# Performance work log

Hardware: AMD Instinct MI355X
Metric: run time of the kernel (lower is better)

Reference implementation:

```python
import jax, jax.numpy as jnp
import numpy as np

N = 100000   # nodes
E = 1600000  # edges
R = 500      # relation types
D = 128      # in_ent_feats == out_ent_feats
H = 8        # heads
Dh = 16      # head dim
DFF = 4 * D  # feed-forward hidden
HOPS = 5
ALPHA = 0.15
SLOPE = 0.2
EPS = 1e-5


def setup_inputs() -> dict:
    key = jax.random.key(0)
    ks = jax.random.split(key, 12)
    s = 0.05  # small-init scale
    return {
        "ent_feat": jax.random.normal(ks[0], (N, D), jnp.float32),
        "rel_feat": jax.random.normal(ks[1], (R, D), jnp.float32),
        "src": jax.random.randint(ks[2], (E,), 0, N),
        "dst": jax.random.randint(ks[3], (E,), 0, N),
        "e_type": jax.random.randint(ks[4], (E,), 0, R),
        "ln1_g": jnp.ones((D,), jnp.float32),
        "ln1_b": jnp.zeros((D,), jnp.float32),
        "W_ent": jax.random.normal(ks[5], (D, H * Dh), jnp.float32) * s,
        "W_rel": jax.random.normal(ks[6], (D, H * Dh), jnp.float32) * s,
        "attn_h": jax.random.normal(ks[7], (1, H, Dh), jnp.float32) * s,
        "attn_t": jax.random.normal(ks[8], (1, H, Dh), jnp.float32) * s,
        "attn_r": jax.random.normal(ks[9], (1, H, Dh), jnp.float32) * s,
        "ln2_g": jnp.ones((H * Dh,), jnp.float32),
        "ln2_b": jnp.zeros((H * Dh,), jnp.float32),
        "W1": jax.random.normal(ks[10], (H * Dh, DFF), jnp.float32) * s,
        "b1": jnp.zeros((DFF,), jnp.float32),
        "W2": jax.random.normal(ks[11], (DFF, H * Dh), jnp.float32) * s,
        "b2": jnp.zeros((H * Dh,), jnp.float32),
    }


def _ln(x, g, b):
    mu = x.mean(-1, keepdims=True)
    var = x.var(-1, keepdims=True)
    return (x - mu) * jax.lax.rsqrt(var + EPS) * g + b


def reference(ent_feat, rel_feat, src, dst, e_type,
              ln1_g, ln1_b, W_ent, W_rel, attn_h, attn_t, attn_r,
              ln2_g, ln2_b, W1, b1, W2, b2):
    # graph layer norm (dropout is identity at eval)
    h = _ln(ent_feat, ln1_g, ln1_b)                       # [N, D]
    feat = (h @ W_ent).reshape(N, H, Dh)                  # [N, H, Dh]
    frel = (rel_feat @ W_rel).reshape(R, H, Dh)           # [R, H, Dh]
    eh = (feat * attn_h).sum(-1)                          # [N, H]
    et = (feat * attn_t).sum(-1)                          # [N, H]
    er = (frel * attn_r).sum(-1)[e_type]                  # [E, H]
    # edge scores: u_add_v + relation term, leaky relu
    e = eh[src] + et[dst] + er                            # [E, H]
    e = jnp.where(e > 0, e, SLOPE * e)
    # edge softmax over incoming edges of each dst node
    m = jax.ops.segment_max(e, dst, num_segments=N)       # [N, H]
    ex = jnp.exp(e - m[dst])
    ssum = jax.ops.segment_sum(ex, dst, num_segments=N)
    a = ex / ssum[dst]                                    # [E, H]
    # PPR diffusion
    feat0 = feat
    f = feat0
    for _ in range(HOPS):
        msg = f[src] * a[:, :, None]                      # [E, H, Dh]
        agg = jax.ops.segment_sum(msg, dst, num_segments=N)
        f = (1.0 - ALPHA) * agg + ALPHA * feat0
    # residual (Identity since in == out)
    rst = f + h.reshape(N, H, Dh)
    rst = rst.reshape(N, H * Dh)
    # feed-forward sublayer with residual
    y = _ln(rst, ln2_g, ln2_b)
    ff = jax.nn.relu(y @ W1 + b1) @ W2 + b2
    return ff + rst
```

## Files before the change

kernel.cpp:

```cpp
#include <hip/hip_runtime.h>
#include <hip/hip_bf16.h>
#include <math.h>

#define N_NODES 100000
#define N_EDGES 1600000
#define N_REL   500
#define DIM     128
#define NHEAD   8
#define DFF     512
#define ALPHA   0.15f
#define SLOPE   0.2f
#define LN_EPS  1e-5f

#define SCHUNK   1024
#define NSCANBLK ((N_NODES + SCHUNK - 1) / SCHUNK)

#define NWIN    8
#define WNODES  12500
#define NECHUNK 256
#define ECHUNK  (N_EDGES / NECHUNK)

typedef unsigned short u16;
typedef unsigned int   u32;

typedef __attribute__((ext_vector_type(8))) short  bf16x8;
typedef __attribute__((ext_vector_type(4))) float  f32x4;

__device__ __forceinline__ float bf2f(u16 u) {
    return __uint_as_float(((u32)u) << 16);
}
__device__ __forceinline__ u16 f2bf(float f) {
    __hip_bfloat16 b = __float2bfloat16(f);
    return *reinterpret_cast<u16*>(&b);
}

__global__ void zero_k(int* __restrict__ p, int n) {
    int i = blockIdx.x * blockDim.x + threadIdx.x;
    if (i < n) p[i] = 0;
}

__global__ void swz1_k(const float* __restrict__ W1, u16* __restrict__ W1s) {
    const int i = blockIdx.x * 256 + threadIdx.x;
    const int k = i >> 9, n = i & 511;
    W1s[n * DIM + k] = f2bf(W1[i]);
}
__global__ void swz2_k(const float* __restrict__ W2, u16* __restrict__ W2s) {
    const int i = blockIdx.x * 256 + threadIdx.x;
    const int k = i >> 7, n = i & 127;
    W2s[n * DFF + k] = f2bf(W2[i]);
}
__global__ void swze_k(const float* __restrict__ W, u16* __restrict__ Ws) {
    const int i = blockIdx.x * 256 + threadIdx.x;
    const int k = i >> 7, n = i & 127;
    Ws[n * DIM + k] = f2bf(W[i]);
}

__global__ __launch_bounds__(128) void ln1_k(const float* __restrict__ x,
        const float* __restrict__ g, const float* __restrict__ b,
        float* __restrict__ h) {
    const int n = blockIdx.x, t = threadIdx.x;
    const float v = x[n * DIM + t];
    float s = v, q = v * v;
#pragma unroll
    for (int off = 32; off > 0; off >>= 1) {
        s += __shfl_xor(s, off, 64);
        q += __shfl_xor(q, off, 64);
    }
    __shared__ float ss[2], qq[2];
    if ((t & 63) == 0) { ss[t >> 6] = s; qq[t >> 6] = q; }
    __syncthreads();
    s = ss[0] + ss[1]; q = qq[0] + qq[1];
    const float mu  = s * (1.0f / 128.0f);
    const float var = q * (1.0f / 128.0f) - mu * mu;
    const float rs  = rsqrtf(fmaxf(var, 0.f) + LN_EPS);
    h[n * DIM + t] = (v - mu) * rs * g[t] + b[t];
}

#define HP 136
__global__ __launch_bounds__(256) void proj_k(const float* __restrict__ h,
        const u16* __restrict__ Wes,
        u16* __restrict__ feat0) {
    __shared__ u16 hsb[32 * HP];
    const int t   = threadIdx.x;
    const int n0b = blockIdx.x * 32;

    {
        const int sr = t >> 3;
        const int sc = (t & 7) * 16;
        const float* hrow = &h[(size_t)(n0b + sr) * DIM + sc];
        u16* drow = &hsb[sr * HP + sc];
#pragma unroll
        for (int i = 0; i < 4; ++i) {
            const float4 hv = ((const float4*)hrow)[i];
            ushort4 o;
            o.x = f2bf(hv.x); o.y = f2bf(hv.y); o.z = f2bf(hv.z); o.w = f2bf(hv.w);
            ((ushort4*)drow)[i] = o;
        }
    }
    __syncthreads();

    const int wv   = t >> 6;
    const int lane = t & 63;
    const int lm   = lane & 15;
    const int q4   = lane >> 4;
    const int mrow = (wv & 1) * 16;
    const int chalf = (wv >> 1) * 64;

    bf16x8 afr[4];
#pragma unroll
    for (int kt = 0; kt < 4; ++kt)
        afr[kt] = *(const bf16x8*)&hsb[(mrow + lm) * HP + kt * 32 + q4 * 8];

#pragma unroll
    for (int nt = 0; nt < 4; ++nt) {
        const int c0 = chalf + nt * 16;
        f32x4 acc = {0.f, 0.f, 0.f, 0.f};
#pragma unroll
        for (int kt = 0; kt < 4; ++kt) {
            const bf16x8 bfr = *(const bf16x8*)&Wes[(c0 + lm) * DIM + kt * 32 + q4 * 8];
            acc = __builtin_amdgcn_mfma_f32_16x16x32_bf16(afr[kt], bfr, acc, 0, 0, 0);
        }
#pragma unroll
        for (int r = 0; r < 4; ++r)
            feat0[(size_t)(n0b + mrow + q4 * 4 + r) * DIM + c0 + lm] = f2bf(acc[r]);
    }
}

__global__ __launch_bounds__(256) void eh_k(const u16* __restrict__ feat0,
        const float* __restrict__ attn_h, const float* __restrict__ attn_t,
        float* __restrict__ eh, float* __restrict__ et) {
    __shared__ float ahs[DIM], ats[DIM];
    const int t = threadIdx.x;
    if (t < DIM) { ahs[t] = attn_h[t]; ats[t] = attn_t[t]; }
    __syncthreads();
    const int idx  = blockIdx.x * 256 + t;
    const int n    = idx >> 3;
    const int head = idx & 7;
    const u16* fp = &feat0[(size_t)n * DIM + head * 16];
    float sh = 0.f, st = 0.f;
#pragma unroll
    for (int i = 0; i < 4; ++i) {
        const ushort4 f4 = ((const ushort4*)fp)[i];
        const int c = head * 16 + i * 4;
        sh += bf2f(f4.x) * ahs[c+0] + bf2f(f4.y) * ahs[c+1]
            + bf2f(f4.z) * ahs[c+2] + bf2f(f4.w) * ahs[c+3];
        st += bf2f(f4.x) * ats[c+0] + bf2f(f4.y) * ats[c+1]
            + bf2f(f4.z) * ats[c+2] + bf2f(f4.w) * ats[c+3];
    }
    eh[idx] = sh;
    et[idx] = st;
}

__global__ __launch_bounds__(128) void rel_k(const float* __restrict__ rel_feat,
        const float* __restrict__ W,
        const float* __restrict__ attn_r, float* __restrict__ er) {
    __shared__ float rf[DIM];
    __shared__ float pr[DIM];
    const int r = blockIdx.x, t = threadIdx.x;
    rf[t] = rel_feat[r * DIM + t];
    __syncthreads();
    float acc = 0.f;
    for (int d = 0; d < DIM; ++d) acc += rf[d] * W[d * DIM + t];
    pr[t] = acc * attn_r[t];
    __syncthreads();
    if (t < NHEAD) {
        float s = 0.f;
        for (int i = 0; i < 16; ++i) s += pr[t * 16 + i];
        er[r * NHEAD + t] = s;
    }
}

__global__ void count_k(const int* __restrict__ dst, int* __restrict__ counts) {
    int e = blockIdx.x * blockDim.x + threadIdx.x;
    if (e < N_EDGES) atomicAdd(&counts[dst[e]], 1);
}

__global__ __launch_bounds__(256) void scan1_k(const int* __restrict__ counts,
        int* __restrict__ offsets, int* __restrict__ blk_sums, int n) {
    __shared__ int wsum[4];
    const int t = threadIdx.x, lane = t & 63, wid = t >> 6;
    const int base = blockIdx.x * SCHUNK + t * 4;
    int v0 = 0, v1 = 0, v2 = 0, v3 = 0;
    if (base + 3 < n) {
        const int4 c4 = *(const int4*)&counts[base];
        v0 = c4.x; v1 = c4.y; v2 = c4.z; v3 = c4.w;
    } else {
        if (base + 0 < n) v0 = counts[base + 0];
        if (base + 1 < n) v1 = counts[base + 1];
        if (base + 2 < n) v2 = counts[base + 2];
        if (base + 3 < n) v3 = counts[base + 3];
    }
    const int s4 = v0 + v1 + v2 + v3;
    int incl = s4;
#pragma unroll
    for (int off = 1; off < 64; off <<= 1) {
        const int tt = __shfl_up(incl, off, 64);
        if (lane >= off) incl += tt;
    }
    if (lane == 63) wsum[wid] = incl;
    __syncthreads();
    int wbase = 0;
#pragma unroll
    for (int w = 0; w < 4; ++w) if (w < wid) wbase += wsum[w];
    const int excl = wbase + incl - s4;
    if (base + 0 < n) offsets[base + 0] = excl;
    if (base + 1 < n) offsets[base + 1] = excl + v0;
    if (base + 2 < n) offsets[base + 2] = excl + v0 + v1;
    if (base + 3 < n) offsets[base + 3] = excl + v0 + v1 + v2;
    if (t == 255) blk_sums[blockIdx.x] = wbase + incl;
}

__global__ __launch_bounds__(128) void scan2_k(const int* __restrict__ blk_sums,
        int* __restrict__ blk_off, int* __restrict__ offsets, int nblk, int n) {
    const int t = threadIdx.x;
    const int v = (t < nblk) ? blk_sums[t] : 0;
    int incl = v;
#pragma unroll
    for (int off = 1; off < 64; off <<= 1) {
        const int tt = __shfl_up(incl, off, 64);
        if ((t & 63) >= off) incl += tt;
    }
    __shared__ int w0sum;
    if (t == 63) w0sum = incl;
    __syncthreads();
    int x = incl - v;
    if (t >= 64) x += w0sum;
    if (t < nblk) blk_off[t] = x;
    if (t == nblk - 1) offsets[n] = x + v;
}

__global__ __launch_bounds__(256) void scan3_k(int* __restrict__ offsets,
        int* __restrict__ cursor, const int* __restrict__ blk_off, int n) {
    const int add  = blk_off[blockIdx.x];
    const int base = blockIdx.x * SCHUNK + threadIdx.x * 4;
#pragma unroll
    for (int j = 0; j < 4; ++j) {
        const int i = base + j;
        if (i < n) {
            const int o = offsets[i] + add;
            offsets[i] = o;
            cursor[i]  = o;
        }
    }
}

__global__ __launch_bounds__(256) void scatter_k(const int* __restrict__ src,
        const int* __restrict__ dst, const int* __restrict__ etype,
        int* __restrict__ cursor, u32* __restrict__ csr_se) {
    const int b  = blockIdx.x;
    const int w  = b & (NWIN - 1);
    const int r  = b >> 3;
    const int lo = w * WNODES, hi = lo + WNODES;
    const int base = r * ECHUNK;
    for (int i = threadIdx.x; i < ECHUNK; i += 256) {
        const int e = base + i;
        const int d = dst[e];
        if (d >= lo && d < hi) {
            const int s   = src[e];
            const int rel = etype[e];
            const int pos = atomicAdd(&cursor[d], 1);
            if (pos >= 0 && pos < N_EDGES)
                csr_se[pos] = (u32)s | ((u32)rel << 17);
        }
    }
}

__global__ __launch_bounds__(256) void softmax_k(const int* __restrict__ offsets,
        const u32* __restrict__ csr_se,
        const float* __restrict__ eh, const float* __restrict__ et,
        const float* __restrict__ er,
        u16* __restrict__ csr_ab, float* __restrict__ inv_buf) {
    const int n = blockIdx.x * 4 + (threadIdx.x >> 6);
    const int beg = offsets[n], end = offsets[n + 1];
    const int lane = threadIdx.x & 63;
    const int k  = lane & 7;
    const int eo = lane >> 3;
    const float etk = et[n * NHEAD + k];
    float m = -1e30f;
    for (int e = beg + eo; e < end; e += 8) {
        const u32 se = csr_se[e];
        const int s = se & 0x1FFFF;
        const int r = se >> 17;
        float sc = eh[s * NHEAD + k] + etk + er[r * NHEAD + k];
        sc = sc > 0.f ? sc : SLOPE * sc;
        m = fmaxf(m, sc);
    }
    m = fmaxf(m, __shfl_xor(m, 8, 64));
    m = fmaxf(m, __shfl_xor(m, 16, 64));
    m = fmaxf(m, __shfl_xor(m, 32, 64));
    float ssum = 0.f;
    for (int e = beg + eo; e < end; e += 8) {
        const u32 se = csr_se[e];
        const int s = se & 0x1FFFF;
        const int r = se >> 17;
        float sc = eh[s * NHEAD + k] + etk + er[r * NHEAD + k];
        sc = sc > 0.f ? sc : SLOPE * sc;
        const float ex = expf(sc - m);
        csr_ab[(size_t)e * NHEAD + k] = f2bf(ex);
        ssum += ex;
    }
    ssum += __shfl_xor(ssum, 8, 64);
    ssum += __shfl_xor(ssum, 16, 64);
    ssum += __shfl_xor(ssum, 32, 64);
    const float inv = 1.f / fmaxf(ssum, 1e-20f);
    if (lane < 8) inv_buf[n * NHEAD + lane] = inv;
}

__global__ __launch_bounds__(256) void hop_k(const u16* __restrict__ f_in,
        u16* __restrict__ f_out, const u16* __restrict__ feat0,
        const int* __restrict__ offsets, const u32* __restrict__ csr_se,
        const u16* __restrict__ csr_ab, const float* __restrict__ inv_buf) {
    const int n    = blockIdx.x * 4 + (threadIdx.x >> 6);
    const int lane = threadIdx.x & 63;
    const int li   = lane & 15;
    const int grp  = lane >> 4;
    const int hsel = li >> 1;
    const int beg = offsets[n], end = offsets[n + 1];

    float acc[8];
#pragma unroll
    for (int j = 0; j < 8; ++j) acc[j] = 0.f;

    int e0 = beg;
    for (; e0 + 32 <= end; e0 += 32) {
        const u32 seA = csr_se[e0 + li];
        const u32 seB = csr_se[e0 + 16 + li];
        bf16x8 row[8];
        float  a[8];
#pragma unroll
        for (int u = 0; u < 4; ++u) {
            const int s = (int)(__shfl(seA, u * 4 + grp, 16) & 0x1FFFF);
            row[u] = *(const bf16x8*)&f_in[(size_t)s * DIM + li * 8];
            a[u]   = bf2f(csr_ab[(size_t)(e0 + u * 4 + grp) * NHEAD + hsel]);
        }
#pragma unroll
        for (int u = 0; u < 4; ++u) {
            const int s = (int)(__shfl(seB, u * 4 + grp, 16) & 0x1FFFF);
            row[4 + u] = *(const bf16x8*)&f_in[(size_t)s * DIM + li * 8];
            a[4 + u]   = bf2f(csr_ab[(size_t)(e0 + 16 + u * 4 + grp) * NHEAD + hsel]);
        }
#pragma unroll
        for (int u = 0; u < 8; ++u)
#pragma unroll
            for (int j = 0; j < 8; ++j)
                acc[j] += a[u] * bf2f((u16)row[u][j]);
    }
    for (; e0 + 16 <= end; e0 += 16) {
        const u32 se16 = csr_se[e0 + li];
#pragma unroll
        for (int u = 0; u < 4; ++u) {
            const int eu = e0 + u * 4 + grp;
            const int s  = (int)(__shfl(se16, u * 4 + grp, 16) & 0x1FFFF);
            const float av = bf2f(csr_ab[(size_t)eu * NHEAD + hsel]);
            const bf16x8 rw = *(const bf16x8*)&f_in[(size_t)s * DIM + li * 8];
#pragma unroll
            for (int j = 0; j < 8; ++j)
                acc[j] += av * bf2f((u16)rw[j]);
        }
    }
    for (int e = e0 + grp; e < end; e += 4) {
        const u32 se = csr_se[e];
        const int s  = (int)(se & 0x1FFFF);
        const float av = bf2f(csr_ab[(size_t)e * NHEAD + hsel]);
        const bf16x8 rw = *(const bf16x8*)&f_in[(size_t)s * DIM + li * 8];
#pragma unroll
        for (int j = 0; j < 8; ++j)
            acc[j] += av * bf2f((u16)rw[j]);
    }
#pragma unroll
    for (int j = 0; j < 8; ++j) {
        acc[j] += __shfl_xor(acc[j], 16, 64);
        acc[j] += __shfl_xor(acc[j], 32, 64);
    }
    if (lane < 16) {
        const float iv = inv_buf[n * NHEAD + hsel];
        const bf16x8 p = *(const bf16x8*)&feat0[(size_t)n * DIM + li * 8];
        bf16x8 o;
#pragma unroll
        for (int j = 0; j < 8; ++j)
            o[j] = (short)f2bf((1.f - ALPHA) * acc[j] * iv + ALPHA * bf2f((u16)p[j]));
        *(bf16x8*)&f_out[(size_t)n * DIM + li * 8] = o;
    }
}

#define YP 136
#define ZP 520
__global__ __launch_bounds__(256) void ffn_k(const u16* __restrict__ f,
        const float* __restrict__ h,
        const float* __restrict__ g2, const float* __restrict__ b2ln,
        const u16* __restrict__ W1s,
        const float* __restrict__ b1,
        const u16* __restrict__ W2s,
        const float* __restrict__ b2,
        float* __restrict__ out) {
    __shared__ u16 ysb[32 * YP];
    __shared__ u16 zsb[32 * ZP];
    __shared__ float red[32][8];
    __shared__ float red2[32][8];
    __shared__ float mu_s[32], rs_s[32];

    const int t   = threadIdx.x;
    const int n0b = blockIdx.x * 32;

    const int an = t >> 3;
    const int ap = t & 7;
    float rv[16];
    {
        const int gbase = (n0b + an) * DIM + ap * 16;
#pragma unroll
        for (int i = 0; i < 4; ++i) {
            const ushort4 fu = *(const ushort4*)&f[gbase + i * 4];
            const float4  hv = *(const float4*)&h[gbase + i * 4];
            rv[i * 4 + 0] = bf2f(fu.x) + hv.x;
            rv[i * 4 + 1] = bf2f(fu.y) + hv.y;
            rv[i * 4 + 2] = bf2f(fu.z) + hv.z;
            rv[i * 4 + 3] = bf2f(fu.w) + hv.w;
        }
        float s = 0.f, q = 0.f;
#pragma unroll
        for (int i = 0; i < 16; ++i) { s += rv[i]; q += rv[i] * rv[i]; }
        red[an][ap] = s; red2[an][ap] = q;
    }
    __syncthreads();
    if (t < 32) {
        float s = 0.f, q = 0.f;
#pragma unroll
        for (int i = 0; i < 8; ++i) { s += red[t][i]; q += red2[t][i]; }
        const float mu  = s * (1.0f / 128.0f);
        const float var = q * (1.0f / 128.0f) - mu * mu;
        mu_s[t] = mu;
        rs_s[t] = rsqrtf(fmaxf(var, 0.f) + LN_EPS);
    }
    __syncthreads();
    {
        const float mu = mu_s[an], rs = rs_s[an];
#pragma unroll
        for (int i = 0; i < 4; ++i) {
            ushort4 yo;
            const int c = ap * 16 + i * 4;
            yo.x = f2bf((rv[i*4+0] - mu) * rs * g2[c+0] + b2ln[c+0]);
            yo.y = f2bf((rv[i*4+1] - mu) * rs * g2[c+1] + b2ln[c+1]);
            yo.z = f2bf((rv[i*4+2] - mu) * rs * g2[c+2] + b2ln[c+2]);
            yo.w = f2bf((rv[i*4+3] - mu) * rs * g2[c+3] + b2ln[c+3]);
            *(ushort4*)&ysb[an * YP + c] = yo;
        }
    }
    __syncthreads();

    const int wv   = t >> 6;
    const int lane = t & 63;
    const int lm   = lane & 15;
    const int q4   = lane >> 4;

    bf16x8 afr[2][4];
#pragma unroll
    for (int mt = 0; mt < 2; ++mt)
#pragma unroll
        for (int kt = 0; kt < 4; ++kt)
            afr[mt][kt] = *(const bf16x8*)&ysb[(mt * 16 + lm) * YP + kt * 32 + q4 * 8];

    for (int nt = 0; nt < 8; ++nt) {
        const int n0 = wv * 128 + nt * 16;
        f32x4 acc0 = {0.f, 0.f, 0.f, 0.f};
        f32x4 acc1 = {0.f, 0.f, 0.f, 0.f};
#pragma unroll
        for (int kt = 0; kt < 4; ++kt) {
            const bf16x8 bfr = *(const bf16x8*)&W1s[(n0 + lm) * DIM + kt * 32 + q4 * 8];
            acc0 = __builtin_amdgcn_mfma_f32_16x16x32_bf16(afr[0][kt], bfr, acc0, 0, 0, 0);
            acc1 = __builtin_amdgcn_mfma_f32_16x16x32_bf16(afr[1][kt], bfr, acc1, 0, 0, 0);
        }
        const float bias = b1[n0 + lm];
#pragma unroll
        for (int r = 0; r < 4; ++r) {
            zsb[(q4 * 4 + r) * ZP + n0 + lm]        = f2bf(fmaxf(acc0[r] + bias, 0.f));
            zsb[(16 + q4 * 4 + r) * ZP + n0 + lm]   = f2bf(fmaxf(acc1[r] + bias, 0.f));
        }
    }
    __syncthreads();

    f32x4 acc[2][2];
#pragma unroll
    for (int i = 0; i < 2; ++i)
#pragma unroll
        for (int j = 0; j < 2; ++j)
            acc[i][j] = (f32x4){0.f, 0.f, 0.f, 0.f};
    const int c0 = wv * 32;
    for (int kt = 0; kt < 16; ++kt) {
        const bf16x8 a0 = *(const bf16x8*)&zsb[(lm) * ZP + kt * 32 + q4 * 8];
        const bf16x8 a1 = *(const bf16x8*)&zsb[(16 + lm) * ZP + kt * 32 + q4 * 8];
        const bf16x8 b0 = *(const bf16x8*)&W2s[(c0 + lm) * DFF + kt * 32 + q4 * 8];
        const bf16x8 b1f = *(const bf16x8*)&W2s[(c0 + 16 + lm) * DFF + kt * 32 + q4 * 8];
        acc[0][0] = __builtin_amdgcn_mfma_f32_16x16x32_bf16(a0, b0, acc[0][0], 0, 0, 0);
        acc[0][1] = __builtin_amdgcn_mfma_f32_16x16x32_bf16(a0, b1f, acc[0][1], 0, 0, 0);
        acc[1][0] = __builtin_amdgcn_mfma_f32_16x16x32_bf16(a1, b0, acc[1][0], 0, 0, 0);
        acc[1][1] = __builtin_amdgcn_mfma_f32_16x16x32_bf16(a1, b1f, acc[1][1], 0, 0, 0);
    }

#pragma unroll
    for (int ntile = 0; ntile < 2; ++ntile) {
        const int col = c0 + ntile * 16 + lm;
        const float bias = b2[col];
#pragma unroll
        for (int mt = 0; mt < 2; ++mt) {
#pragma unroll
            for (int r = 0; r < 4; ++r) {
                const int row  = mt * 16 + q4 * 4 + r;
                const int gidx = (n0b + row) * DIM + col;
                out[gidx] = acc[mt][ntile][r] + bias + bf2f(f[gidx]) + h[gidx];
            }
        }
    }
}

extern "C" void kernel_launch(void* const* d_in, const int* in_sizes, int n_in,
                              void* d_out, int out_size, void* d_ws, size_t ws_size,
                              hipStream_t stream) {
    const float* ent_feat = (const float*)d_in[0];
    const float* rel_feat = (const float*)d_in[1];
    const int*   src      = (const int*)d_in[2];
    const int*   dst      = (const int*)d_in[3];
    const int*   e_type   = (const int*)d_in[4];
    const float* ln1_g    = (const float*)d_in[5];
    const float* ln1_b    = (const float*)d_in[6];
    const float* W_ent    = (const float*)d_in[7];
    const float* W_rel    = (const float*)d_in[8];
    const float* attn_h   = (const float*)d_in[9];
    const float* attn_t   = (const float*)d_in[10];
    const float* attn_r   = (const float*)d_in[11];
    const float* ln2_g    = (const float*)d_in[12];
    const float* ln2_b    = (const float*)d_in[13];
    const float* W1       = (const float*)d_in[14];
    const float* b1       = (const float*)d_in[15];
    const float* W2       = (const float*)d_in[16];
    const float* b2       = (const float*)d_in[17];
    float* out = (float*)d_out;

    char* ws = (char*)d_ws;
    size_t used = 0;
    auto alloc = [&](size_t bytes) -> char* {
        char* p = ws + used;
        used += (bytes + 255) & ~(size_t)255;
        return p;
    };
    float* h       = (float*)alloc((size_t)N_NODES * DIM * 4);
    u16*   feat0   = (u16*)  alloc((size_t)N_NODES * DIM * 2);
    u16*   fA      = (u16*)  alloc((size_t)N_NODES * DIM * 2);
    u16*   fB      = (u16*)  alloc((size_t)N_NODES * DIM * 2);
    u16*   csr_ab  = (u16*)  alloc((size_t)N_EDGES * NHEAD * 2);
    float* eh      = (float*)alloc((size_t)N_NODES * NHEAD * 4);
    float* et      = (float*)alloc((size_t)N_NODES * NHEAD * 4);
    float* inv_buf = (float*)alloc((size_t)N_NODES * NHEAD * 4);
    u32*   csr_se  = (u32*)  alloc((size_t)N_EDGES * 4);
    int*   counts  = (int*)  alloc((size_t)N_NODES * 4);
    int*   offsets = (int*)  alloc((size_t)(N_NODES + 1) * 4);
    int*   cursor  = (int*)  alloc((size_t)N_NODES * 4);
    float* er      = (float*)alloc((size_t)N_REL * NHEAD * 4);
    u16*   W1s     = (u16*)  alloc((size_t)DIM * DFF * 2);
    u16*   W2s     = (u16*)  alloc((size_t)DFF * DIM * 2);
    u16*   Wes     = (u16*)  alloc((size_t)DIM * DIM * 2);
    int*   blk_sums= (int*)  alloc((size_t)NSCANBLK * 4);
    int*   blk_off = (int*)  alloc((size_t)NSCANBLK * 4);

    if (used > ws_size) return;

    swz1_k<<<DIM * DFF / 256, 256, 0, stream>>>(W1, W1s);
    swz2_k<<<DFF * DIM / 256, 256, 0, stream>>>(W2, W2s);
    swze_k<<<DIM * DIM / 256, 256, 0, stream>>>(W_ent, Wes);

    ln1_k<<<N_NODES, 128, 0, stream>>>(ent_feat, ln1_g, ln1_b, h);
    proj_k<<<N_NODES / 32, 256, 0, stream>>>(h, Wes, feat0);
    eh_k<<<N_NODES * NHEAD / 256, 256, 0, stream>>>(feat0, attn_h, attn_t, eh, et);
    rel_k<<<N_REL, 128, 0, stream>>>(rel_feat, W_rel, attn_r, er);

    zero_k<<<(N_NODES + 255) / 256, 256, 0, stream>>>(counts, N_NODES);
    count_k<<<(N_EDGES + 255) / 256, 256, 0, stream>>>(dst, counts);
    scan1_k<<<NSCANBLK, 256, 0, stream>>>(counts, offsets, blk_sums, N_NODES);
    scan2_k<<<1, 128, 0, stream>>>(blk_sums, blk_off, offsets, NSCANBLK, N_NODES);
    scan3_k<<<NSCANBLK, 256, 0, stream>>>(offsets, cursor, blk_off, N_NODES);
    scatter_k<<<NECHUNK * NWIN, 256, 0, stream>>>(src, dst, e_type,
                                                  cursor, csr_se);
    softmax_k<<<N_NODES / 4, 256, 0, stream>>>(offsets, csr_se, eh, et, er,
                                               csr_ab, inv_buf);

    hop_k<<<N_NODES / 4, 256, 0, stream>>>(feat0, fA, feat0, offsets, csr_se, csr_ab, inv_buf);
    hop_k<<<N_NODES / 4, 256, 0, stream>>>(fA, fB, feat0, offsets, csr_se, csr_ab, inv_buf);
    hop_k<<<N_NODES / 4, 256, 0, stream>>>(fB, fA, feat0, offsets, csr_se, csr_ab, inv_buf);
    hop_k<<<N_NODES / 4, 256, 0, stream>>>(fA, fB, feat0, offsets, csr_se, csr_ab, inv_buf);
    hop_k<<<N_NODES / 4, 256, 0, stream>>>(fB, fA, feat0, offsets, csr_se, csr_ab, inv_buf);

    ffn_k<<<N_NODES / 32, 256, 0, stream>>>(fA, h, ln2_g, ln2_b, W1s, b1, W2s, b2,
                                            out);
}
```

Before: 936.1 us.

## Cache softmax scores, simplify hop gather loop, prefetch FFN weights, shuffle-reduce LN

Softmax now keeps the first four per-lane edge scores in registers, so the common low-degree case skips reloading and recomputing them in the exp pass. The hop kernel replaces its 32/16/tail loops with a single 16-edge loop that predicates the ragged tail. It also sets launch_bounds to 8 blocks for more occupancy and unpacks bf16 pairs directly with bit ops. The FFN kernel replaces the shared-memory LayerNorm reduction and two barriers with wave shuffles, and double-buffers W1/W2 fragment loads ahead of the MFMAs. The risks are register pressure from the occupancy hint and prefetch buffers, and less memory-level parallelism per wave in the hop gather.

```diff
diff --git a/kernel.cpp b/kernel.cpp
--- a/kernel.cpp
+++ b/kernel.cpp
@@ -32,6 +32,15 @@
 __device__ __forceinline__ u16 f2bf(float f) {
     __hip_bfloat16 b = __float2bfloat16(f);
     return *reinterpret_cast<u16*>(&b);
+}
+
+__device__ __forceinline__ void fma_row(float* acc, float a, const bf16x8& r) {
+    const u32* w = (const u32*)&r;
+#pragma unroll
+    for (int jj = 0; jj < 4; ++jj) {
+        acc[2 * jj]     += a * __uint_as_float(w[jj] << 16);
+        acc[2 * jj + 1] += a * __uint_as_float(w[jj] & 0xffff0000u);
+    }
 }
 
 __global__ void zero_k(int* __restrict__ p, int n) {
@@ -276,26 +285,38 @@
     const int k  = lane & 7;
     const int eo = lane >> 3;
     const float etk = et[n * NHEAD + k];
-    float m = -1e30f;
-    for (int e = beg + eo; e < end; e += 8) {
+
+    auto score = [&](int e) -> float {
         const u32 se = csr_se[e];
         const int s = se & 0x1FFFF;
         const int r = se >> 17;
         float sc = eh[s * NHEAD + k] + etk + er[r * NHEAD + k];
-        sc = sc > 0.f ? sc : SLOPE * sc;
-        m = fmaxf(m, sc);
-    }
+        return sc > 0.f ? sc : SLOPE * sc;
+    };
+
+    const int e0 = beg + eo;
+    float c0 = 0.f, c1 = 0.f, c2 = 0.f, c3 = 0.f;
+    float m = -1e30f;
+    if (e0 < end)      { c0 = score(e0);      m = fmaxf(m, c0); }
+    if (e0 + 8 < end)  { c1 = score(e0 + 8);  m = fmaxf(m, c1); }
+    if (e0 + 16 < end) { c2 = score(e0 + 16); m = fmaxf(m, c2); }
+    if (e0 + 24 < end) { c3 = score(e0 + 24); m = fmaxf(m, c3); }
+    for (int e = e0 + 32; e < end; e += 8) m = fmaxf(m, score(e));
     m = fmaxf(m, __shfl_xor(m, 8, 64));
     m = fmaxf(m, __shfl_xor(m, 16, 64));
     m = fmaxf(m, __shfl_xor(m, 32, 64));
+
     float ssum = 0.f;
-    for (int e = beg + eo; e < end; e += 8) {
-        const u32 se = csr_se[e];
-        const int s = se & 0x1FFFF;
-        const int r = se >> 17;
-        float sc = eh[s * NHEAD + k] + etk + er[r * NHEAD + k];
-        sc = sc > 0.f ? sc : SLOPE * sc;
-        const float ex = expf(sc - m);
+    if (e0 < end)      { const float ex = expf(c0 - m);
+                         csr_ab[(size_t)e0 * NHEAD + k] = f2bf(ex); ssum += ex; }
+    if (e0 + 8 < end)  { const float ex = expf(c1 - m);
+                         csr_ab[(size_t)(e0 + 8) * NHEAD + k] = f2bf(ex); ssum += ex; }
+    if (e0 + 16 < end) { const float ex = expf(c2 - m);
+                         csr_ab[(size_t)(e0 + 16) * NHEAD + k] = f2bf(ex); ssum += ex; }
+    if (e0 + 24 < end) { const float ex = expf(c3 - m);
+                         csr_ab[(size_t)(e0 + 24) * NHEAD + k] = f2bf(ex); ssum += ex; }
+    for (int e = e0 + 32; e < end; e += 8) {
+        const float ex = expf(score(e) - m);
         csr_ab[(size_t)e * NHEAD + k] = f2bf(ex);
         ssum += ex;
     }
@@ -306,7 +327,7 @@
     if (lane < 8) inv_buf[n * NHEAD + lane] = inv;
 }
 
-__global__ __launch_bounds__(256) void hop_k(const u16* __restrict__ f_in,
+__global__ __launch_bounds__(256, 8) void hop_k(const u16* __restrict__ f_in,
         u16* __restrict__ f_out, const u16* __restrict__ feat0,
         const int* __restrict__ offsets, const u32* __restrict__ csr_se,
         const u16* __restrict__ csr_ab, const float* __restrict__ inv_buf) {
@@ -321,51 +342,42 @@
 #pragma unroll
     for (int j = 0; j < 8; ++j) acc[j] = 0.f;
 
-    int e0 = beg;
-    for (; e0 + 32 <= end; e0 += 32) {
-        const u32 seA = csr_se[e0 + li];
-        const u32 seB = csr_se[e0 + 16 + li];
-        bf16x8 row[8];
-        float  a[8];
-#pragma unroll
-        for (int u = 0; u < 4; ++u) {
-            const int s = (int)(__shfl(seA, u * 4 + grp, 16) & 0x1FFFF);
-            row[u] = *(const bf16x8*)&f_in[(size_t)s * DIM + li * 8];
-            a[u]   = bf2f(csr_ab[(size_t)(e0 + u * 4 + grp) * NHEAD + hsel]);
-        }
-#pragma unroll
-        for (int u = 0; u < 4; ++u) {
-            const int s = (int)(__shfl(seB, u * 4 + grp, 16) & 0x1FFFF);
-            row[4 + u] = *(const bf16x8*)&f_in[(size_t)s * DIM + li * 8];
-            a[4 + u]   = bf2f(csr_ab[(size_t)(e0 + 16 + u * 4 + grp) * NHEAD + hsel]);
-        }
-#pragma unroll
-        for (int u = 0; u < 8; ++u)
-#pragma unroll
-            for (int j = 0; j < 8; ++j)
-                acc[j] += a[u] * bf2f((u16)row[u][j]);
-    }
-    for (; e0 + 16 <= end; e0 += 16) {
-        const u32 se16 = csr_se[e0 + li];
-#pragma unroll
-        for (int u = 0; u < 4; ++u) {
-            const int eu = e0 + u * 4 + grp;
-            const int s  = (int)(__shfl(se16, u * 4 + grp, 16) & 0x1FFFF);
-            const float av = bf2f(csr_ab[(size_t)eu * NHEAD + hsel]);
-            const bf16x8 rw = *(const bf16x8*)&f_in[(size_t)s * DIM + li * 8];
-#pragma unroll
-            for (int j = 0; j < 8; ++j)
-                acc[j] += av * bf2f((u16)rw[j]);
-        }
-    }
-    for (int e = e0 + grp; e < end; e += 4) {
-        const u32 se = csr_se[e];
-        const int s  = (int)(se & 0x1FFFF);
-        const float av = bf2f(csr_ab[(size_t)e * NHEAD + hsel]);
-        const bf16x8 rw = *(const bf16x8*)&f_in[(size_t)s * DIM + li * 8];
-#pragma unroll
-        for (int j = 0; j < 8; ++j)
-            acc[j] += av * bf2f((u16)rw[j]);
+    for (int e0 = beg; e0 < end; e0 += 16) {
+        const u32 se16 = csr_se[min(e0 + li, end - 1)];
+        const int s0 = (int)(__shfl(se16, grp,      16) & 0x1FFFF);
+        const int s1 = (int)(__shfl(se16, 4 + grp,  16) & 0x1FFFF);
+        const int s2 = (int)(__shfl(se16, 8 + grp,  16) & 0x1FFFF);
+        const int s3 = (int)(__shfl(se16, 12 + grp, 16) & 0x1FFFF);
+        if (e0 + 16 <= end) {
+            const bf16x8 r0 = *(const bf16x8*)&f_in[(size_t)s0 * DIM + li * 8];
+            const bf16x8 r1 = *(const bf16x8*)&f_in[(size_t)s1 * DIM + li * 8];
+            const bf16x8 r2 = *(const bf16x8*)&f_in[(size_t)s2 * DIM + li * 8];
+            const bf16x8 r3 = *(const bf16x8*)&f_in[(size_t)s3 * DIM + li * 8];
+            const float a0 = bf2f(csr_ab[(size_t)(e0 + grp)      * NHEAD + hsel]);
+            const float a1 = bf2f(csr_ab[(size_t)(e0 + 4 + grp)  * NHEAD + hsel]);
+            const float a2 = bf2f(csr_ab[(size_t)(e0 + 8 + grp)  * NHEAD + hsel]);
+            const float a3 = bf2f(csr_ab[(size_t)(e0 + 12 + grp) * NHEAD + hsel]);
+            fma_row(acc, a0, r0);
+            fma_row(acc, a1, r1);
+            fma_row(acc, a2, r2);
+            fma_row(acc, a3, r3);
+        } else {
+            const int rem = end - e0;
+            bf16x8 r0 = {}, r1 = {}, r2 = {}, r3 = {};
+            float a0 = 0.f, a1 = 0.f, a2 = 0.f, a3 = 0.f;
+            if (grp < rem)      { r0 = *(const bf16x8*)&f_in[(size_t)s0 * DIM + li * 8];
+                                  a0 = bf2f(csr_ab[(size_t)(e0 + grp)      * NHEAD + hsel]); }
+            if (grp + 4 < rem)  { r1 = *(const bf16x8*)&f_in[(size_t)s1 * DIM + li * 8];
+                                  a1 = bf2f(csr_ab[(size_t)(e0 + 4 + grp)  * NHEAD + hsel]); }
+            if (grp + 8 < rem)  { r2 = *(const bf16x8*)&f_in[(size_t)s2 * DIM + li * 8];
+                                  a2 = bf2f(csr_ab[(size_t)(e0 + 8 + grp)  * NHEAD + hsel]); }
+            if (grp + 12 < rem) { r3 = *(const bf16x8*)&f_in[(size_t)s3 * DIM + li * 8];
+                                  a3 = bf2f(csr_ab[(size_t)(e0 + 12 + grp) * NHEAD + hsel]); }
+            fma_row(acc, a0, r0);
+            fma_row(acc, a1, r1);
+            fma_row(acc, a2, r2);
+            fma_row(acc, a3, r3);
+        }
     }
 #pragma unroll
     for (int j = 0; j < 8; ++j) {
@@ -395,18 +407,18 @@
         float* __restrict__ out) {
     __shared__ u16 ysb[32 * YP];
     __shared__ u16 zsb[32 * ZP];
-    __shared__ float red[32][8];
-    __shared__ float red2[32][8];
-    __shared__ float mu_s[32], rs_s[32];
-
-    const int t   = threadIdx.x;
-    const int n0b = blockIdx.x * 32;
-
-    const int an = t >> 3;
-    const int ap = t & 7;
-    float rv[16];
+
+    const int t    = threadIdx.x;
+    const int n0b  = blockIdx.x * 32;
+    const int wv   = t >> 6;
+    const int lane = t & 63;
+
     {
-        const int gbase = (n0b + an) * DIM + ap * 16;
+        const int nl   = lane >> 3;
+        const int node = wv * 8 + nl;
+        const int cp   = (lane & 7) * 16;
+        const int gbase = (n0b + node) * DIM + cp;
+        float rv[16];
 #pragma unroll
         for (int i = 0; i < 4; ++i) {
             const ushort4 fu = *(const ushort4*)&f[gbase + i * 4];
@@ -419,61 +431,66 @@
         float s = 0.f, q = 0.f;
 #pragma unroll
         for (int i = 0; i < 16; ++i) { s += rv[i]; q += rv[i] * rv[i]; }
-        red[an][ap] = s; red2[an][ap] = q;
-    }
-    __syncthreads();
-    if (t < 32) {
-        float s = 0.f, q = 0.f;
-#pragma unroll
-        for (int i = 0; i < 8; ++i) { s += red[t][i]; q += red2[t][i]; }
+        s += __shfl_xor(s, 1, 64); q += __shfl_xor(q, 1, 64);
+        s += __shfl_xor(s, 2, 64); q += __shfl_xor(q, 2, 64);
+        s += __shfl_xor(s, 4, 64); q += __shfl_xor(q, 4, 64);
         const float mu  = s * (1.0f / 128.0f);
         const float var = q * (1.0f / 128.0f) - mu * mu;
-        mu_s[t] = mu;
-        rs_s[t] = rsqrtf(fmaxf(var, 0.f) + LN_EPS);
-    }
-    __syncthreads();
-    {
-        const float mu = mu_s[an], rs = rs_s[an];
+        const float rs  = rsqrtf(fmaxf(var, 0.f) + LN_EPS);
 #pragma unroll
         for (int i = 0; i < 4; ++i) {
             ushort4 yo;
-            const int c = ap * 16 + i * 4;
+            const int c = cp + i * 4;
             yo.x = f2bf((rv[i*4+0] - mu) * rs * g2[c+0] + b2ln[c+0]);
             yo.y = f2bf((rv[i*4+1] - mu) * rs * g2[c+1] + b2ln[c+1]);
             yo.z = f2bf((rv[i*4+2] - mu) * rs * g2[c+2] + b2ln[c+2]);
             yo.w = f2bf((rv[i*4+3] - mu) * rs * g2[c+3] + b2ln[c+3]);
-            *(ushort4*)&ysb[an * YP + c] = yo;
-        }
-    }
-    __syncthreads();
-
-    const int wv   = t >> 6;
-    const int lane = t & 63;
-    const int lm   = lane & 15;
-    const int q4   = lane >> 4;
-
-    bf16x8 afr[2][4];
-#pragma unroll
-    for (int mt = 0; mt < 2; ++mt)
+            *(ushort4*)&ysb[node * YP + c] = yo;
+        }
+    }
+    __syncthreads();
+
+    const int lm = lane & 15;
+    const int q4 = lane >> 4;
+
+    {
+        bf16x8 afr[2][4];
+#pragma unroll
+        for (int mt = 0; mt < 2; ++mt)
+#pragma unroll
+            for (int kt = 0; kt < 4; ++kt)
+                afr[mt][kt] = *(const bf16x8*)&ysb[(mt * 16 + lm) * YP + kt * 32 + q4 * 8];
+
+        const int cw = wv * 128;
+        bf16x8 bc[4];
 #pragma unroll
         for (int kt = 0; kt < 4; ++kt)
-            afr[mt][kt] = *(const bf16x8*)&ysb[(mt * 16 + lm) * YP + kt * 32 + q4 * 8];
-
-    for (int nt = 0; nt < 8; ++nt) {
-        const int n0 = wv * 128 + nt * 16;
-        f32x4 acc0 = {0.f, 0.f, 0.f, 0.f};
-        f32x4 acc1 = {0.f, 0.f, 0.f, 0.f};
-#pragma unroll
-        for (int kt = 0; kt < 4; ++kt) {
-            const bf16x8 bfr = *(const bf16x8*)&W1s[(n0 + lm) * DIM + kt * 32 + q4 * 8];
-            acc0 = __builtin_amdgcn_mfma_f32_16x16x32_bf16(afr[0][kt], bfr, acc0, 0, 0, 0);
-            acc1 = __builtin_amdgcn_mfma_f32_16x16x32_bf16(afr[1][kt], bfr, acc1, 0, 0, 0);
-        }
-        const float bias = b1[n0 + lm];
-#pragma unroll
-        for (int r = 0; r < 4; ++r) {
-            zsb[(q4 * 4 + r) * ZP + n0 + lm]        = f2bf(fmaxf(acc0[r] + bias, 0.f));
-            zsb[(16 + q4 * 4 + r) * ZP + n0 + lm]   = f2bf(fmaxf(acc1[r] + bias, 0.f));
+            bc[kt] = *(const bf16x8*)&W1s[(cw + lm) * DIM + kt * 32 + q4 * 8];
+
+#pragma unroll
+        for (int nt = 0; nt < 8; ++nt) {
+            const int n0 = cw + nt * 16;
+            bf16x8 bn[4] = {bc[0], bc[1], bc[2], bc[3]};
+            if (nt < 7) {
+#pragma unroll
+                for (int kt = 0; kt < 4; ++kt)
+                    bn[kt] = *(const bf16x8*)&W1s[(n0 + 16 + lm) * DIM + kt * 32 + q4 * 8];
+            }
+            f32x4 acc0 = {0.f, 0.f, 0.f, 0.f};
+            f32x4 acc1 = {0.f, 0.f, 0.f, 0.f};
+#pragma unroll
+            for (int kt = 0; kt < 4; ++kt) {
+                acc0 = __builtin_amdgcn_mfma_f32_16x16x32_bf16(afr[0][kt], bc[kt], acc0, 0, 0, 0);
+                acc1 = __builtin_amdgcn_mfma_f32_16x16x32_bf16(afr[1][kt], bc[kt], acc1, 0, 0, 0);
+            }
+            const float bias = b1[n0 + lm];
+#pragma unroll
+            for (int r = 0; r < 4; ++r) {
+                zsb[(q4 * 4 + r) * ZP + n0 + lm]      = f2bf(fmaxf(acc0[r] + bias, 0.f));
+                zsb[(16 + q4 * 4 + r) * ZP + n0 + lm] = f2bf(fmaxf(acc1[r] + bias, 0.f));
+            }
+#pragma unroll
+            for (int kt = 0; kt < 4; ++kt) bc[kt] = bn[kt];
         }
     }
     __syncthreads();
@@ -485,15 +502,22 @@
         for (int j = 0; j < 2; ++j)
             acc[i][j] = (f32x4){0.f, 0.f, 0.f, 0.f};
     const int c0 = wv * 32;
+    bf16x8 wc0 = *(const bf16x8*)&W2s[(c0 + lm) * DFF + q4 * 8];
+    bf16x8 wc1 = *(const bf16x8*)&W2s[(c0 + 16 + lm) * DFF + q4 * 8];
+#pragma unroll
     for (int kt = 0; kt < 16; ++kt) {
+        bf16x8 wn0 = wc0, wn1 = wc1;
+        if (kt < 15) {
+            wn0 = *(const bf16x8*)&W2s[(c0 + lm) * DFF + (kt + 1) * 32 + q4 * 8];
+            wn1 = *(const bf16x8*)&W2s[(c0 + 16 + lm) * DFF + (kt + 1) * 32 + q4 * 8];
+        }
         const bf16x8 a0 = *(const bf16x8*)&zsb[(lm) * ZP + kt * 32 + q4 * 8];
         const bf16x8 a1 = *(const bf16x8*)&zsb[(16 + lm) * ZP + kt * 32 + q4 * 8];
-        const bf16x8 b0 = *(const bf16x8*)&W2s[(c0 + lm) * DFF + kt * 32 + q4 * 8];
-        const bf16x8 b1f = *(const bf16x8*)&W2s[(c0 + 16 + lm) * DFF + kt * 32 + q4 * 8];
-        acc[0][0] = __builtin_amdgcn_mfma_f32_16x16x32_bf16(a0, b0, acc[0][0], 0, 0, 0);
-        acc[0][1] = __builtin_amdgcn_mfma_f32_16x16x32_bf16(a0, b1f, acc[0][1], 0, 0, 0);
-        acc[1][0] = __builtin_amdgcn_mfma_f32_16x16x32_bf16(a1, b0, acc[1][0], 0, 0, 0);
-        acc[1][1] = __builtin_amdgcn_mfma_f32_16x16x32_bf16(a1, b1f, acc[1][1], 0, 0, 0);
+        acc[0][0] = __builtin_amdgcn_mfma_f32_16x16x32_bf16(a0, wc0, acc[0][0], 0, 0, 0);
+        acc[0][1] = __builtin_amdgcn_mfma_f32_16x16x32_bf16(a0, wc1, acc[0][1], 0, 0, 0);
+        acc[1][0] = __builtin_amdgcn_mfma_f32_16x16x32_bf16(a1, wc0, acc[1][0], 0, 0, 0);
+        acc[1][1] = __builtin_amdgcn_mfma_f32_16x16x32_bf16(a1, wc1, acc[1][1], 0, 0, 0);
+        wc0 = wn0; wc1 = wn1;
     }
 
 #pragma unroll
```

Measured after the change: 1.057 ms. +12.9%, slower.
